# Kernel optimization log

Hardware: AMD Instinct MI355X
Metric: run time of the kernel (lower is better)

The kernel has to match this reference:

```python
import jax, jax.numpy as jnp
import numpy as np

DIM = 1024
NUM_EXPERTS = 8
TOP_K = 2
HIDDEN = int(2 * 4 * DIM / 3)  # 2730, SwiGLU hidden dim


def setup_inputs() -> dict:
    key = jax.random.key(0)
    ks = jax.random.split(key, 5)
    s = 0.02
    return {
        "x": jax.random.normal(ks[0], (2, 2048, DIM), dtype=jnp.float32),
        "router_w": jax.random.normal(ks[1], (DIM, NUM_EXPERTS), dtype=jnp.float32) * s,
        "w_gate": jax.random.normal(ks[2], (NUM_EXPERTS, DIM, HIDDEN), dtype=jnp.float32) * s,
        "w_up": jax.random.normal(ks[3], (NUM_EXPERTS, DIM, HIDDEN), dtype=jnp.float32) * s,
        "w_down": jax.random.normal(ks[4], (NUM_EXPERTS, HIDDEN, DIM), dtype=jnp.float32) * s,
    }


def reference(x, router_w, w_gate, w_up, w_down):
    B, S, D = x.shape
    xf = x.reshape(-1, D)  # [T, D]

    router_logits = xf @ router_w  # [T, E]
    topk_logits, topk_idx = jax.lax.top_k(router_logits, TOP_K)  # [T, K]
    routing_weights = jax.nn.softmax(topk_logits, axis=-1)  # [T, K]

    # Scatter top-k weights into dense [T, E] combine weights (0 for unselected
    # experts) -> mathematically identical to the per-expert gather/scatter loop.
    combine = (jax.nn.one_hot(topk_idx, NUM_EXPERTS, dtype=xf.dtype)
               * routing_weights[..., None]).sum(axis=1)  # [T, E]

    # SwiGLU experts computed for all tokens, weighted combine.
    gate = jax.nn.silu(jnp.einsum('td,edh->eth', xf, w_gate))  # [E, T, H]
    up = jnp.einsum('td,edh->eth', xf, w_up)                   # [E, T, H]
    expert_out = jnp.einsum('eth,ehd->etd', gate * up, w_down)  # [E, T, D]
    out = jnp.einsum('te,etd->td', combine, expert_out).reshape(B, S, D)

    # Auxiliary losses
    router_probs = jax.nn.softmax(router_logits, axis=-1)
    expert_usage = router_probs.mean(axis=0)
    load_balance_loss = NUM_EXPERTS * jnp.sum(expert_usage ** 2)
    router_z_loss = jnp.mean(jax.nn.logsumexp(router_logits, axis=-1) ** 2)
    return out, load_balance_loss, router_z_loss
```

## Files before the change

### kernel.cpp

```cpp
#include <hip/hip_runtime.h>
#include <cstdint>
#include <cstddef>

#define T_TOK 4096
#define DIM   1024
#define NEXP  8
#define HID   2730
#define HP2   2816
#define NB1   5632
#define NPAIR (T_TOK*2)

typedef __attribute__((ext_vector_type(8))) short short8;
typedef __attribute__((ext_vector_type(4))) float f32x4;

#define OFF_CNT   0UL
#define OFF_USE   64UL
#define OFF_Z     96UL
#define OFF_OFFS  160UL
#define OFF_LIST  256UL
#define OFF_PAIRW 131328UL
#define OFF_XB    164096UL
#define OFF_H     (OFF_XB + 8388608UL)
#define OFF_B2    (OFF_H + 46137344UL)
#define OFF_B1    (OFF_B2 + 46137344UL)
#define OFF_OP    OFF_B1

__device__ __forceinline__ unsigned short f2bf(float f) {
    unsigned u = __float_as_uint(f);
    return (unsigned short)((u + 0x7FFFu + ((u >> 16) & 1u)) >> 16);
}

__device__ __forceinline__ unsigned pack2(float a, float b) {
    return (unsigned)f2bf(a) | ((unsigned)f2bf(b) << 16);
}

__device__ __forceinline__ void load_lds16(const void* g, void* l) {
    __builtin_amdgcn_global_load_lds(
        (const __attribute__((address_space(1))) void*)g,
        (__attribute__((address_space(3))) void*)l, 16, 0, 0);
}

struct __align__(8) us4 { unsigned short x, y, z, w; };
struct __align__(8) u32x2 { unsigned x, y; };

__global__ __launch_bounds__(256) void router_kernel(
    const float* __restrict__ x, const float* __restrict__ rw,
    int* __restrict__ counts, float* __restrict__ usage, float* __restrict__ zacc,
    int* __restrict__ lists, float* __restrict__ pairw,
    unsigned short* __restrict__ xb)
{
    __shared__ float s_rw[NEXP][DIM];
    __shared__ float s_use[NEXP];
    __shared__ float s_z;
    const int tid = threadIdx.x;
    for (int i = tid; i < DIM * NEXP; i += 256) s_rw[i & 7][i >> 3] = rw[i];
    if (tid < NEXP) s_use[tid] = 0.f;
    if (tid == NEXP) s_z = 0.f;
    __syncthreads();

    const int wave = tid >> 6, lane = tid & 63;
    const int t = blockIdx.x * 4 + wave;

    float acc[NEXP];
    #pragma unroll
    for (int e = 0; e < NEXP; ++e) acc[e] = 0.f;
    #pragma unroll
    for (int j = 0; j < DIM / 64; ++j) {
        const int d = j * 64 + lane;
        const float xv = x[(size_t)t * DIM + d];
        xb[(size_t)t * DIM + d] = f2bf(xv);
        #pragma unroll
        for (int e = 0; e < NEXP; ++e) acc[e] = fmaf(xv, s_rw[e][d], acc[e]);
    }
    #pragma unroll
    for (int e = 0; e < NEXP; ++e) {
        float v = acc[e];
        for (int off = 32; off > 0; off >>= 1) v += __shfl_down(v, off, 64);
        acc[e] = v;
    }
    if (lane == 0) {
        float l[NEXP];
        #pragma unroll
        for (int e = 0; e < NEXP; ++e) l[e] = acc[e];
        float m = l[0];
        #pragma unroll
        for (int e = 1; e < NEXP; ++e) m = fmaxf(m, l[e]);
        float se = 0.f;
        #pragma unroll
        for (int e = 0; e < NEXP; ++e) se += __expf(l[e] - m);
        const float lse = m + __logf(se);
        #pragma unroll
        for (int e = 0; e < NEXP; ++e) atomicAdd(&s_use[e], __expf(l[e] - m) / se);
        atomicAdd(&s_z, lse * lse);
        int i0 = 0; float l0 = l[0];
        #pragma unroll
        for (int e = 1; e < NEXP; ++e) if (l[e] > l0) { l0 = l[e]; i0 = e; }
        int i1 = -1; float l1 = -1e30f;
        #pragma unroll
        for (int e = 0; e < NEXP; ++e) if (e != i0 && l[e] > l1) { l1 = l[e]; i1 = e; }
        const float p0 = 1.f / (1.f + __expf(l1 - l0));
        const float p1 = 1.f - p0;
        const int pos0 = atomicAdd(&counts[i0], 1);
        lists[i0 * T_TOK + pos0] = (t << 1);
        const int pos1 = atomicAdd(&counts[i1], 1);
        lists[i1 * T_TOK + pos1] = (t << 1) | 1;
        pairw[2 * t]     = p0;
        pairw[2 * t + 1] = p1;
    }
    __syncthreads();
    if (tid < NEXP) atomicAdd(&usage[tid], s_use[tid]);
    if (tid == NEXP) atomicAdd(zacc, s_z);
}

__global__ void finalize_kernel(const int* __restrict__ counts,
                                const float* __restrict__ usage,
                                const float* __restrict__ zacc,
                                int* __restrict__ offs,
                                float* __restrict__ out)
{
    if (threadIdx.x == 0 && blockIdx.x == 0) {
        int o = 0;
        for (int e = 0; e < NEXP; ++e) { offs[e] = o; o += counts[e]; }
        float s = 0.f;
        for (int e = 0; e < NEXP; ++e) {
            const float u = usage[e] / (float)T_TOK;
            s += u * u;
        }
        out[(size_t)T_TOK * DIM]     = (float)NEXP * s;
        out[(size_t)T_TOK * DIM + 1] = zacc[0] / (float)T_TOK;
    }
}

__global__ __launch_bounds__(256) void conv_w1_kernel(
    const float* __restrict__ wg, const float* __restrict__ wu,
    unsigned short* __restrict__ B1)
{
    __shared__ unsigned short lg[128 * 128];
    __shared__ unsigned short lu[128 * 128];
    const int e = blockIdx.z;
    const int h0 = blockIdx.x * 128;
    const int k0 = blockIdx.y * 128;
    const int tid = threadIdx.x;
    const size_t wb = (size_t)e * DIM * HID;

    const int hu = (tid & 31) * 4;
    const int kg = tid >> 5;
    const bool full = (h0 + 128 <= HID);

    #pragma unroll
    for (int uu = 0; uu < 4; ++uu) {
        const int kk = (kg * 4 + uu) * 4;
        f32x4 g[4], u[4];
        if (full) {
            #pragma unroll
            for (int j = 0; j < 4; ++j) {
                const size_t src = wb + (size_t)(k0 + kk + j) * HID + h0 + hu;
                g[j] = *(const f32x4*)&wg[src];
                u[j] = *(const f32x4*)&wu[src];
            }
        } else {
            #pragma unroll
            for (int j = 0; j < 4; ++j) {
                #pragma unroll
                for (int c = 0; c < 4; ++c) {
                    const int hh = h0 + hu + c;
                    float gv = 0.f, uv = 0.f;
                    if (hh < HID) {
                        const size_t src = wb + (size_t)(k0 + kk + j) * HID + hh;
                        gv = wg[src]; uv = wu[src];
                    }
                    g[j][c] = gv; u[j][c] = uv;
                }
            }
        }
        #pragma unroll
        for (int i = 0; i < 4; ++i) {
            const int h = hu + i;
            const int byte = (((h * 128 + kk) * 2) ^ ((h & 15) << 4));
            u32x2 vg; vg.x = pack2(g[0][i], g[1][i]); vg.y = pack2(g[2][i], g[3][i]);
            u32x2 vu; vu.x = pack2(u[0][i], u[1][i]); vu.y = pack2(u[2][i], u[3][i]);
            *(u32x2*)((char*)lg + byte) = vg;
            *(u32x2*)((char*)lu + byte) = vu;
        }
    }
    __syncthreads();

    const int kc  = (tid & 15) * 8;
    const int hrb = tid >> 4;
    #pragma unroll
    for (int wo = 0; wo < 8; ++wo) {
        const int h = hrb + wo * 16;
        const int byte = (((h * 128 + kc) * 2) ^ ((h & 15) << 4));
        const short8 vg = *(const short8*)((const char*)lg + byte);
        const short8 vu = *(const short8*)((const char*)lu + byte);
        *(short8*)&B1[((size_t)e * NB1 + h0 + h) * DIM + k0 + kc] = vg;
        *(short8*)&B1[((size_t)e * NB1 + HP2 + h0 + h) * DIM + k0 + kc] = vu;
    }
}

__global__ __launch_bounds__(256) void conv_w2_kernel(
    const float* __restrict__ wd, unsigned short* __restrict__ B2)
{
    __shared__ unsigned short lw[128 * 128];
    const int e = blockIdx.z;
    const int h0 = blockIdx.x * 128;
    const int d0 = blockIdx.y * 128;
    const int tid = threadIdx.x;
    const size_t wb = (size_t)e * HID * DIM;

    const int du = (tid & 31) * 4;
    const int kg = tid >> 5;

    #pragma unroll
    for (int uu = 0; uu < 4; ++uu) {
        const int kk = (kg * 4 + uu) * 4;
        f32x4 v[4];
        #pragma unroll
        for (int j = 0; j < 4; ++j) {
            const int hh = h0 + kk + j;
            if (hh < HID) v[j] = *(const f32x4*)&wd[wb + (size_t)hh * DIM + d0 + du];
            else          v[j] = (f32x4)0.f;
        }
        #pragma unroll
        for (int i = 0; i < 4; ++i) {
            const int d = du + i;
            const int byte = (((d * 128 + kk) * 2) ^ ((d & 15) << 4));
            u32x2 vv; vv.x = pack2(v[0][i], v[1][i]); vv.y = pack2(v[2][i], v[3][i]);
            *(u32x2*)((char*)lw + byte) = vv;
        }
    }
    __syncthreads();

    const int kc  = (tid & 15) * 8;
    const int drb = tid >> 4;
    #pragma unroll
    for (int wo = 0; wo < 8; ++wo) {
        const int d = drb + wo * 16;
        const int byte = (((d * 128 + kc) * 2) ^ ((d & 15) << 4));
        const short8 vv = *(const short8*)((const char*)lw + byte);
        *(short8*)&B2[((size_t)e * DIM + d0 + d) * HP2 + h0 + kc] = vv;
    }
}

__global__ __launch_bounds__(256, 2) void gemm1_kernel(
    const unsigned short* __restrict__ xb, const unsigned short* __restrict__ B1,
    const int* __restrict__ counts, const int* __restrict__ offs,
    const int* __restrict__ lists, unsigned short* __restrict__ h)
{
    const int e = blockIdx.z;
    const int cnt = counts[e];
    int wg = blockIdx.x + 22 * blockIdx.y;
    wg = (wg & 7) * 88 + (wg >> 3);
    const int by = wg & 31;
    const int bx = wg >> 5;
    const int row0 = by * 128;
    if (row0 >= cnt) return;
    const int off = offs[e];
    const int n0 = bx * 128;

    __shared__ unsigned short s1[24576];
    __shared__ int s_pr[128];

    const int tid = threadIdx.x;
    const int w = tid >> 6, lane = tid & 63;
    if (tid < 128) {
        const int r = row0 + tid;
        s_pr[tid] = (r < cnt) ? lists[e * T_TOK + r] : -1;
    }
    __syncthreads();

    const int rA = tid >> 2, kb = tid & 3;
    const int kbs = (kb ^ ((rA >> 1) & 3)) * 8;
    const int pr0 = s_pr[rA], pr1 = s_pr[rA + 64];
    const unsigned short* agp0 = xb + (size_t)(max(pr0, 0) >> 1) * DIM + kbs;
    const unsigned short* agp1 = xb + (size_t)(max(pr1, 0) >> 1) * DIM + kbs;
    const unsigned short* bgp0 = B1 + ((size_t)e * NB1 + n0 + rA) * DIM + kbs;
    const unsigned short* bgp1 = bgp0 + (size_t)64 * DIM;
    const unsigned short* bup0 = B1 + ((size_t)e * NB1 + HP2 + n0 + rA) * DIM + kbs;
    const unsigned short* bup1 = bup0 + (size_t)64 * DIM;

    char* const s1b = (char*)s1;
    const int sw = w * 1024;

    f32x4 accg[4][4], accu[4][4];
    #pragma unroll
    for (int i = 0; i < 4; ++i)
        #pragma unroll
        for (int j = 0; j < 4; ++j) { accg[i][j] = (f32x4)0.f; accu[i][j] = (f32x4)0.f; }

    const int wm = w & 1, wn = w >> 1;
    const int fm = lane & 15, fq = lane >> 4;
    const int kq = (fq ^ ((fm >> 1) & 3)) * 8;

    auto STAGE = [&](char* base, int k0) {
        load_lds16(agp0 + k0, base + sw);
        load_lds16(agp1 + k0, base + 4096 + sw);
        load_lds16(bgp0 + k0, base + 8192 + sw);
        load_lds16(bgp1 + k0, base + 12288 + sw);
        load_lds16(bup0 + k0, base + 16384 + sw);
        load_lds16(bup1 + k0, base + 20480 + sw);
    };
    auto COMPUTE = [&](const unsigned short* bufA) {
        const unsigned short* bufG = bufA + 4096;
        const unsigned short* bufU = bufA + 8192;
        short8 a[4], bg[4], bu[4];
        #pragma unroll
        for (int i = 0; i < 4; ++i) {
            a[i]  = *(const short8*)&bufA[(wm * 64 + i * 16 + fm) * 32 + kq];
            bg[i] = *(const short8*)&bufG[(wn * 64 + i * 16 + fm) * 32 + kq];
            bu[i] = *(const short8*)&bufU[(wn * 64 + i * 16 + fm) * 32 + kq];
        }
        __builtin_amdgcn_s_setprio(1);
        #pragma unroll
        for (int i = 0; i < 4; ++i)
            #pragma unroll
            for (int j = 0; j < 4; ++j) {
                accg[i][j] = __builtin_amdgcn_mfma_f32_16x16x32_bf16(a[i], bg[j], accg[i][j], 0, 0, 0);
                accu[i][j] = __builtin_amdgcn_mfma_f32_16x16x32_bf16(a[i], bu[j], accu[i][j], 0, 0, 0);
            }
        __builtin_amdgcn_s_setprio(0);
    };

    STAGE(s1b, 0);
    __syncthreads();
    #pragma unroll 1
    for (int g = 0; g < 16; ++g) {
        STAGE(s1b + 24576, g * 64 + 32);
        COMPUTE(s1);
        __syncthreads();
        if (g < 15) STAGE(s1b, g * 64 + 64);
        COMPUTE(s1 + 12288);
        __syncthreads();
    }

    unsigned short* wbuf = s1 + w * 1152;
    const int rrow = lane >> 2, cq = (lane & 3) * 16;
    #pragma unroll
    for (int i = 0; i < 4; ++i) {
        #pragma unroll
        for (int j = 0; j < 4; ++j)
            #pragma unroll
            for (int reg = 0; reg < 4; ++reg) {
                const float g = accg[i][j][reg];
                const float u = accu[i][j][reg];
                const float s = g / (1.f + __expf(-g));
                wbuf[(fq * 4 + reg) * 72 + j * 16 + fm] = f2bf(s * u);
            }
        const int rl = wm * 64 + i * 16 + rrow;
        if (row0 + rl < cnt) {
            unsigned short* dst = h + (size_t)(off + row0 + rl) * HP2 + n0 + wn * 64 + cq;
            const short8 v0 = *(const short8*)&wbuf[rrow * 72 + cq];
            const short8 v1 = *(const short8*)&wbuf[rrow * 72 + cq + 8];
            *(short8*)dst = v0;
            *(short8*)(dst + 8) = v1;
        }
    }
}

__global__ __launch_bounds__(256, 2) void gemm2_kernel(
    const unsigned short* __restrict__ h, const unsigned short* __restrict__ B2,
    const int* __restrict__ counts, const int* __restrict__ offs,
    const int* __restrict__ lists, unsigned short* __restrict__ op)
{
    const int e = blockIdx.z;
    const int cnt = counts[e];
    int wg = blockIdx.x + 8 * blockIdx.y;
    wg = (wg & 7) * 32 + (wg >> 3);
    const int by = wg & 31;
    const int bx = wg >> 5;
    const int row0 = by * 128;
    if (row0 >= cnt) return;
    const int off = offs[e];
    const int n0 = bx * 128;

    __shared__ unsigned short s2[32768];
    __shared__ int s_pr[128];

    const int tid = threadIdx.x;
    const int w = tid >> 6, lane = tid & 63;
    if (tid < 128) {
        const int r = row0 + tid;
        s_pr[tid] = (r < cnt) ? lists[e * T_TOK + r] : -1;
    }
    __syncthreads();

    const int rA = tid >> 2, kb = tid & 3;
    const int kbs = (kb ^ ((rA >> 1) & 3)) * 8;
    const unsigned short* agp0 = h + (size_t)(off + row0 + rA) * HP2 + kbs;
    const unsigned short* agp1 = agp0 + (size_t)64 * HP2;
    const unsigned short* bp0 = B2 + ((size_t)e * DIM + n0 + rA) * HP2 + kbs;
    const unsigned short* bp1 = bp0 + (size_t)64 * HP2;

    char* const s2b = (char*)s2;
    const int sw = w * 1024;

    f32x4 acc[4][4];
    #pragma unroll
    for (int i = 0; i < 4; ++i)
        #pragma unroll
        for (int j = 0; j < 4; ++j) acc[i][j] = (f32x4)0.f;

    const int wm = w & 1, wn = w >> 1;
    const int fm = lane & 15, fq = lane >> 4;
    const int kq = (fq ^ ((fm >> 1) & 3)) * 8;

    auto STAGE = [&](char* base, int k0) {
        load_lds16(agp0 + k0,      base + sw);
        load_lds16(agp1 + k0,      base + 4096 + sw);
        load_lds16(agp0 + k0 + 32, base + 8192 + sw);
        load_lds16(agp1 + k0 + 32, base + 12288 + sw);
        load_lds16(bp0 + k0,       base + 16384 + sw);
        load_lds16(bp1 + k0,       base + 20480 + sw);
        load_lds16(bp0 + k0 + 32,  base + 24576 + sw);
        load_lds16(bp1 + k0 + 32,  base + 28672 + sw);
    };
    auto COMPUTE = [&](const unsigned short* buf) {
        #pragma unroll
        for (int hh = 0; hh < 2; ++hh) {
            const unsigned short* bufA = buf + hh * 4096;
            const unsigned short* bufB = buf + 8192 + hh * 4096;
            short8 a[4], bb[4];
            #pragma unroll
            for (int i = 0; i < 4; ++i) {
                a[i]  = *(const short8*)&bufA[(wm * 64 + i * 16 + fm) * 32 + kq];
                bb[i] = *(const short8*)&bufB[(wn * 64 + i * 16 + fm) * 32 + kq];
            }
            __builtin_amdgcn_s_setprio(1);
            #pragma unroll
            for (int i = 0; i < 4; ++i)
                #pragma unroll
                for (int j = 0; j < 4; ++j)
                    acc[i][j] = __builtin_amdgcn_mfma_f32_16x16x32_bf16(a[i], bb[j], acc[i][j], 0, 0, 0);
            __builtin_amdgcn_s_setprio(0);
        }
    };

    STAGE(s2b, 0);
    __syncthreads();
    #pragma unroll 1
    for (int g = 0; g < 22; ++g) {
        STAGE(s2b + 32768, g * 128 + 64);
        COMPUTE(s2);
        __syncthreads();
        if (g < 21) STAGE(s2b, g * 128 + 128);
        COMPUTE(s2 + 16384);
        __syncthreads();
    }

    unsigned short* wbuf = s2 + w * 1152;
    const int rrow = lane >> 2, cq = (lane & 3) * 16;
    #pragma unroll
    for (int i = 0; i < 4; ++i) {
        #pragma unroll
        for (int j = 0; j < 4; ++j)
            #pragma unroll
            for (int reg = 0; reg < 4; ++reg)
                wbuf[(fq * 4 + reg) * 72 + j * 16 + fm] = f2bf(acc[i][j][reg]);
        const int rl = wm * 64 + i * 16 + rrow;
        const int pr = s_pr[rl];
        if (pr >= 0) {
            unsigned short* dst = op + (size_t)pr * DIM + n0 + wn * 64 + cq;
            const short8 v0 = *(const short8*)&wbuf[rrow * 72 + cq];
            const short8 v1 = *(const short8*)&wbuf[rrow * 72 + cq + 8];
            *(short8*)dst = v0;
            *(short8*)(dst + 8) = v1;
        }
    }
}

__global__ __launch_bounds__(256) void combine_kernel(
    const unsigned short* __restrict__ op, const float* __restrict__ pairw,
    float* __restrict__ out)
{
    const int f = blockIdx.x * 256 + threadIdx.x;
    const int t = f >> 8;
    const int c = f & 255;
    const float w0 = pairw[2 * t], w1 = pairw[2 * t + 1];
    const us4 a = ((const us4*)op)[(size_t)(2 * t) * (DIM / 4) + c];
    const us4 b = ((const us4*)op)[(size_t)(2 * t + 1) * (DIM / 4) + c];
    float4 r;
    r.x = w0 * __uint_as_float((unsigned)a.x << 16) + w1 * __uint_as_float((unsigned)b.x << 16);
    r.y = w0 * __uint_as_float((unsigned)a.y << 16) + w1 * __uint_as_float((unsigned)b.y << 16);
    r.z = w0 * __uint_as_float((unsigned)a.z << 16) + w1 * __uint_as_float((unsigned)b.z << 16);
    r.w = w0 * __uint_as_float((unsigned)a.w << 16) + w1 * __uint_as_float((unsigned)b.w << 16);
    ((float4*)out)[f] = r;
}

extern "C" void kernel_launch(void* const* d_in, const int* in_sizes, int n_in,
                              void* d_out, int out_size, void* d_ws, size_t ws_size,
                              hipStream_t stream)
{
    const float* x  = (const float*)d_in[0];
    const float* rw = (const float*)d_in[1];
    const float* wg = (const float*)d_in[2];
    const float* wu = (const float*)d_in[3];
    const float* wd = (const float*)d_in[4];
    float* out = (float*)d_out;
    char* ws = (char*)d_ws;

    int*   counts = (int*)(ws + OFF_CNT);
    float* usage  = (float*)(ws + OFF_USE);
    float* zacc   = (float*)(ws + OFF_Z);
    int*   offs   = (int*)(ws + OFF_OFFS);
    int*   lists  = (int*)(ws + OFF_LIST);
    float* pairw  = (float*)(ws + OFF_PAIRW);
    unsigned short* xb  = (unsigned short*)(ws + OFF_XB);
    unsigned short* hb  = (unsigned short*)(ws + OFF_H);
    unsigned short* B2  = (unsigned short*)(ws + OFF_B2);
    unsigned short* B1  = (unsigned short*)(ws + OFF_B1);
    unsigned short* op  = (unsigned short*)(ws + OFF_OP);

    hipMemsetAsync(ws, 0, 128, stream);

    router_kernel<<<T_TOK / 4, 256, 0, stream>>>(x, rw, counts, usage, zacc, lists, pairw, xb);
    finalize_kernel<<<1, 64, 0, stream>>>(counts, usage, zacc, offs, out);

    conv_w1_kernel<<<dim3(HP2 / 128, DIM / 128, NEXP), 256, 0, stream>>>(wg, wu, B1);
    conv_w2_kernel<<<dim3(HP2 / 128, DIM / 128, NEXP), 256, 0, stream>>>(wd, B2);

    gemm1_kernel<<<dim3(HP2 / 128, T_TOK / 128, NEXP), 256, 0, stream>>>(xb, B1, counts, offs, lists, hb);
    gemm2_kernel<<<dim3(DIM / 128, T_TOK / 128, NEXP), 256, 0, stream>>>(hb, B2, counts, offs, lists, op);

    combine_kernel<<<(T_TOK * DIM / 4) / 256, 256, 0, stream>>>(op, pairw, out);
}
```

Baseline: 628.3 us.

## Triple-buffer gemm2 LDS with K=32 stages and partial vmcnt waits

Restructures the down-projection GEMM main loop from double-buffered 64-wide K stages into a three-buffer ring of 32-wide K stages, shrinking LDS from 64KB to 48KB. Each step waits only for the older stage's loads (vmcnt(4)) before a raw barrier, so one prefetch stays in flight across the barrier. This aims to hide global-load latency better and may allow more resident blocks. In exchange there are more barriers per unit of K work, and correctness depends on the hand-counted vmcnt and the unrolled tail.

```diff
diff --git a/kernel.cpp b/kernel.cpp
--- a/kernel.cpp
+++ b/kernel.cpp
@@ -373,7 +373,7 @@
     const int off = offs[e];
     const int n0 = bx * 128;
 
-    __shared__ unsigned short s2[32768];
+    __shared__ unsigned short s2[24576];
     __shared__ int s_pr[128];
 
     const int tid = threadIdx.x;
@@ -405,47 +405,67 @@
     const int kq = (fq ^ ((fm >> 1) & 3)) * 8;
 
     auto STAGE = [&](char* base, int k0) {
-        load_lds16(agp0 + k0,      base + sw);
-        load_lds16(agp1 + k0,      base + 4096 + sw);
-        load_lds16(agp0 + k0 + 32, base + 8192 + sw);
-        load_lds16(agp1 + k0 + 32, base + 12288 + sw);
-        load_lds16(bp0 + k0,       base + 16384 + sw);
-        load_lds16(bp1 + k0,       base + 20480 + sw);
-        load_lds16(bp0 + k0 + 32,  base + 24576 + sw);
-        load_lds16(bp1 + k0 + 32,  base + 28672 + sw);
+        load_lds16(agp0 + k0, base + sw);
+        load_lds16(agp1 + k0, base + 4096 + sw);
+        load_lds16(bp0 + k0,  base + 8192 + sw);
+        load_lds16(bp1 + k0,  base + 12288 + sw);
     };
-    auto COMPUTE = [&](const unsigned short* buf) {
-        #pragma unroll
-        for (int hh = 0; hh < 2; ++hh) {
-            const unsigned short* bufA = buf + hh * 4096;
-            const unsigned short* bufB = buf + 8192 + hh * 4096;
-            short8 a[4], bb[4];
+    auto COMPUTE = [&](const unsigned short* bufA) {
+        const unsigned short* bufB = bufA + 4096;
+        short8 a[4], bb[4];
+        #pragma unroll
+        for (int i = 0; i < 4; ++i) {
+            a[i]  = *(const short8*)&bufA[(wm * 64 + i * 16 + fm) * 32 + kq];
+            bb[i] = *(const short8*)&bufB[(wn * 64 + i * 16 + fm) * 32 + kq];
+        }
+        __builtin_amdgcn_s_setprio(1);
+        #pragma unroll
+        for (int i = 0; i < 4; ++i)
             #pragma unroll
-            for (int i = 0; i < 4; ++i) {
-                a[i]  = *(const short8*)&bufA[(wm * 64 + i * 16 + fm) * 32 + kq];
-                bb[i] = *(const short8*)&bufB[(wn * 64 + i * 16 + fm) * 32 + kq];
-            }
-            __builtin_amdgcn_s_setprio(1);
-            #pragma unroll
-            for (int i = 0; i < 4; ++i)
-                #pragma unroll
-                for (int j = 0; j < 4; ++j)
-                    acc[i][j] = __builtin_amdgcn_mfma_f32_16x16x32_bf16(a[i], bb[j], acc[i][j], 0, 0, 0);
-            __builtin_amdgcn_s_setprio(0);
-        }
+            for (int j = 0; j < 4; ++j)
+                acc[i][j] = __builtin_amdgcn_mfma_f32_16x16x32_bf16(a[i], bb[j], acc[i][j], 0, 0, 0);
+        __builtin_amdgcn_s_setprio(0);
     };
 
     STAGE(s2b, 0);
-    __syncthreads();
+    STAGE(s2b + 16384, 32);
+    asm volatile("s_waitcnt vmcnt(4)" ::: "memory");
+    __builtin_amdgcn_s_barrier();
+
     #pragma unroll 1
-    for (int g = 0; g < 22; ++g) {
-        STAGE(s2b + 32768, g * 128 + 64);
+    for (int base = 0; base < 84; base += 3) {
+        const int k2 = (base + 2) * 32;
+        STAGE(s2b + 32768, k2);
         COMPUTE(s2);
-        __syncthreads();
-        if (g < 21) STAGE(s2b, g * 128 + 128);
+        asm volatile("s_waitcnt vmcnt(4)" ::: "memory");
+        __builtin_amdgcn_s_barrier();
+
+        STAGE(s2b, k2 + 32);
+        COMPUTE(s2 + 8192);
+        asm volatile("s_waitcnt vmcnt(4)" ::: "memory");
+        __builtin_amdgcn_s_barrier();
+
+        STAGE(s2b + 16384, k2 + 64);
         COMPUTE(s2 + 16384);
-        __syncthreads();
-    }
+        asm volatile("s_waitcnt vmcnt(4)" ::: "memory");
+        __builtin_amdgcn_s_barrier();
+    }
+    STAGE(s2b + 32768, 86 * 32);
+    COMPUTE(s2);
+    asm volatile("s_waitcnt vmcnt(4)" ::: "memory");
+    __builtin_amdgcn_s_barrier();
+
+    STAGE(s2b, 87 * 32);
+    COMPUTE(s2 + 8192);
+    asm volatile("s_waitcnt vmcnt(4)" ::: "memory");
+    __builtin_amdgcn_s_barrier();
+
+    COMPUTE(s2 + 16384);
+    asm volatile("s_waitcnt vmcnt(0)" ::: "memory");
+    __builtin_amdgcn_s_barrier();
+
+    COMPUTE(s2);
+    __builtin_amdgcn_s_barrier();
 
     unsigned short* wbuf = s2 + w * 1152;
     const int rrow = lane >> 2, cq = (lane & 3) * 16;
```

Result: no change. 633.6 us (+0.8%).

## Batch router atomics in shared memory and merge conversion/finalize kernels

Applied to the files above, without the earlier changes.

The router now processes 16 tokens per block, collecting per-expert list entries in shared memory and reserving global slots with one atomic per expert per block instead of per token. The finalize kernel and the two weight-conversion kernels are merged into one launch, with block (0,0,0) doing the offsets and loss finalization. This cuts kernel launches and global atomic contention. The trade-off is fewer router blocks, and the w2 blocks now carry a second, unused LDS buffer, which may lower occupancy.

```diff
diff --git a/kernel.cpp b/kernel.cpp
--- a/kernel.cpp
+++ b/kernel.cpp
@@ -52,73 +52,93 @@
     __shared__ float s_rw[NEXP][DIM];
     __shared__ float s_use[NEXP];
     __shared__ float s_z;
+    __shared__ int   s_cnt[NEXP];
+    __shared__ int   s_base[NEXP];
+    __shared__ int   s_items[NEXP][32];
     const int tid = threadIdx.x;
     for (int i = tid; i < DIM * NEXP; i += 256) s_rw[i & 7][i >> 3] = rw[i];
-    if (tid < NEXP) s_use[tid] = 0.f;
+    if (tid < NEXP) { s_use[tid] = 0.f; s_cnt[tid] = 0; }
     if (tid == NEXP) s_z = 0.f;
     __syncthreads();
 
     const int wave = tid >> 6, lane = tid & 63;
-    const int t = blockIdx.x * 4 + wave;
-
-    float acc[NEXP];
-    #pragma unroll
-    for (int e = 0; e < NEXP; ++e) acc[e] = 0.f;
-    #pragma unroll
-    for (int j = 0; j < DIM / 64; ++j) {
-        const int d = j * 64 + lane;
-        const float xv = x[(size_t)t * DIM + d];
-        xb[(size_t)t * DIM + d] = f2bf(xv);
-        #pragma unroll
-        for (int e = 0; e < NEXP; ++e) acc[e] = fmaf(xv, s_rw[e][d], acc[e]);
-    }
-    #pragma unroll
-    for (int e = 0; e < NEXP; ++e) {
-        float v = acc[e];
-        for (int off = 32; off > 0; off >>= 1) v += __shfl_down(v, off, 64);
-        acc[e] = v;
-    }
-    if (lane == 0) {
-        float l[NEXP];
-        #pragma unroll
-        for (int e = 0; e < NEXP; ++e) l[e] = acc[e];
-        float m = l[0];
-        #pragma unroll
-        for (int e = 1; e < NEXP; ++e) m = fmaxf(m, l[e]);
-        float se = 0.f;
-        #pragma unroll
-        for (int e = 0; e < NEXP; ++e) se += __expf(l[e] - m);
-        const float lse = m + __logf(se);
-        #pragma unroll
-        for (int e = 0; e < NEXP; ++e) atomicAdd(&s_use[e], __expf(l[e] - m) / se);
-        atomicAdd(&s_z, lse * lse);
-        int i0 = 0; float l0 = l[0];
-        #pragma unroll
-        for (int e = 1; e < NEXP; ++e) if (l[e] > l0) { l0 = l[e]; i0 = e; }
-        int i1 = -1; float l1 = -1e30f;
-        #pragma unroll
-        for (int e = 0; e < NEXP; ++e) if (e != i0 && l[e] > l1) { l1 = l[e]; i1 = e; }
-        const float p0 = 1.f / (1.f + __expf(l1 - l0));
-        const float p1 = 1.f - p0;
-        const int pos0 = atomicAdd(&counts[i0], 1);
-        lists[i0 * T_TOK + pos0] = (t << 1);
-        const int pos1 = atomicAdd(&counts[i1], 1);
-        lists[i1 * T_TOK + pos1] = (t << 1) | 1;
-        pairw[2 * t]     = p0;
-        pairw[2 * t + 1] = p1;
-    }
-    __syncthreads();
-    if (tid < NEXP) atomicAdd(&usage[tid], s_use[tid]);
+
+    #pragma unroll 1
+    for (int it = 0; it < 4; ++it) {
+        const int t = blockIdx.x * 16 + wave * 4 + it;
+        float acc[NEXP];
+        #pragma unroll
+        for (int e = 0; e < NEXP; ++e) acc[e] = 0.f;
+        #pragma unroll
+        for (int j = 0; j < DIM / 64; ++j) {
+            const int d = j * 64 + lane;
+            const float xv = x[(size_t)t * DIM + d];
+            xb[(size_t)t * DIM + d] = f2bf(xv);
+            #pragma unroll
+            for (int e = 0; e < NEXP; ++e) acc[e] = fmaf(xv, s_rw[e][d], acc[e]);
+        }
+        #pragma unroll
+        for (int e = 0; e < NEXP; ++e) {
+            float v = acc[e];
+            for (int off = 32; off > 0; off >>= 1) v += __shfl_down(v, off, 64);
+            acc[e] = v;
+        }
+        if (lane == 0) {
+            float l[NEXP];
+            #pragma unroll
+            for (int e = 0; e < NEXP; ++e) l[e] = acc[e];
+            float m = l[0];
+            #pragma unroll
+            for (int e = 1; e < NEXP; ++e) m = fmaxf(m, l[e]);
+            float se = 0.f;
+            #pragma unroll
+            for (int e = 0; e < NEXP; ++e) se += __expf(l[e] - m);
+            const float lse = m + __logf(se);
+            #pragma unroll
+            for (int e = 0; e < NEXP; ++e) atomicAdd(&s_use[e], __expf(l[e] - m) / se);
+            atomicAdd(&s_z, lse * lse);
+            int i0 = 0; float l0 = l[0];
+            #pragma unroll
+            for (int e = 1; e < NEXP; ++e) if (l[e] > l0) { l0 = l[e]; i0 = e; }
+            int i1 = -1; float l1 = -1e30f;
+            #pragma unroll
+            for (int e = 0; e < NEXP; ++e) if (e != i0 && l[e] > l1) { l1 = l[e]; i1 = e; }
+            const float p0 = 1.f / (1.f + __expf(l1 - l0));
+            const float p1 = 1.f - p0;
+            const int pos0 = atomicAdd(&s_cnt[i0], 1);
+            s_items[i0][pos0] = (t << 1);
+            const int pos1 = atomicAdd(&s_cnt[i1], 1);
+            s_items[i1][pos1] = (t << 1) | 1;
+            pairw[2 * t]     = p0;
+            pairw[2 * t + 1] = p1;
+        }
+    }
+    __syncthreads();
+    if (tid < NEXP) {
+        s_base[tid] = atomicAdd(&counts[tid], s_cnt[tid]);
+        atomicAdd(&usage[tid], s_use[tid]);
+    }
     if (tid == NEXP) atomicAdd(zacc, s_z);
-}
-
-__global__ void finalize_kernel(const int* __restrict__ counts,
-                                const float* __restrict__ usage,
-                                const float* __restrict__ zacc,
-                                int* __restrict__ offs,
-                                float* __restrict__ out)
+    __syncthreads();
+    {
+        const int e = tid >> 5, idx = tid & 31;
+        if (idx < s_cnt[e]) lists[e * T_TOK + s_base[e] + idx] = s_items[e][idx];
+    }
+}
+
+__global__ __launch_bounds__(256) void conv_kernel(
+    const float* __restrict__ wg, const float* __restrict__ wu,
+    const float* __restrict__ wd,
+    unsigned short* __restrict__ B1, unsigned short* __restrict__ B2,
+    const int* __restrict__ counts, const float* __restrict__ usage,
+    const float* __restrict__ zacc, int* __restrict__ offs,
+    float* __restrict__ out)
 {
-    if (threadIdx.x == 0 && blockIdx.x == 0) {
+    __shared__ unsigned short lga[128 * 128];
+    __shared__ unsigned short lub[128 * 128];
+    const int tid = threadIdx.x;
+
+    if (blockIdx.x == 0 && blockIdx.y == 0 && blockIdx.z == 0 && tid == 0) {
         int o = 0;
         for (int e = 0; e < NEXP; ++e) { offs[e] = o; o += counts[e]; }
         float s = 0.f;
@@ -129,116 +149,101 @@
         out[(size_t)T_TOK * DIM]     = (float)NEXP * s;
         out[(size_t)T_TOK * DIM + 1] = zacc[0] / (float)T_TOK;
     }
-}
-
-__global__ __launch_bounds__(256) void conv_w1_kernel(
-    const float* __restrict__ wg, const float* __restrict__ wu,
-    unsigned short* __restrict__ B1)
-{
-    __shared__ unsigned short lg[128 * 128];
-    __shared__ unsigned short lu[128 * 128];
-    const int e = blockIdx.z;
-    const int h0 = blockIdx.x * 128;
-    const int k0 = blockIdx.y * 128;
-    const int tid = threadIdx.x;
-    const size_t wb = (size_t)e * DIM * HID;
-
-    const int hu = (tid & 31) * 4;
-    const int kg = tid >> 5;
-    const bool full = (h0 + 128 <= HID);
-
-    #pragma unroll
-    for (int uu = 0; uu < 4; ++uu) {
-        const int kk = (kg * 4 + uu) * 4;
-        f32x4 g[4], u[4];
-        if (full) {
+
+    const int e = blockIdx.z & 7;
+    if (blockIdx.z < 8) {
+        const int h0 = blockIdx.x * 128;
+        const int k0 = blockIdx.y * 128;
+        const size_t wb = (size_t)e * DIM * HID;
+        const int hu = (tid & 31) * 4;
+        const int kg = tid >> 5;
+        const bool full = (h0 + 128 <= HID);
+
+        #pragma unroll
+        for (int uu = 0; uu < 4; ++uu) {
+            const int kk = (kg * 4 + uu) * 4;
+            f32x4 g[4], u[4];
+            if (full) {
+                #pragma unroll
+                for (int j = 0; j < 4; ++j) {
+                    const size_t src = wb + (size_t)(k0 + kk + j) * HID + h0 + hu;
+                    g[j] = *(const f32x4*)&wg[src];
+                    u[j] = *(const f32x4*)&wu[src];
+                }
+            } else {
+                #pragma unroll
+                for (int j = 0; j < 4; ++j) {
+                    #pragma unroll
+                    for (int c = 0; c < 4; ++c) {
+                        const int hh = h0 + hu + c;
+                        float gv = 0.f, uv = 0.f;
+                        if (hh < HID) {
+                            const size_t src = wb + (size_t)(k0 + kk + j) * HID + hh;
+                            gv = wg[src]; uv = wu[src];
+                        }
+                        g[j][c] = gv; u[j][c] = uv;
+                    }
+                }
+            }
+            #pragma unroll
+            for (int i = 0; i < 4; ++i) {
+                const int h = hu + i;
+                const int byte = (((h * 128 + kk) * 2) ^ ((h & 15) << 4));
+                u32x2 vg; vg.x = pack2(g[0][i], g[1][i]); vg.y = pack2(g[2][i], g[3][i]);
+                u32x2 vu; vu.x = pack2(u[0][i], u[1][i]); vu.y = pack2(u[2][i], u[3][i]);
+                *(u32x2*)((char*)lga + byte) = vg;
+                *(u32x2*)((char*)lub + byte) = vu;
+            }
+        }
+        __syncthreads();
+
+        const int kc  = (tid & 15) * 8;
+        const int hrb = tid >> 4;
+        #pragma unroll
+        for (int wo = 0; wo < 8; ++wo) {
+            const int h = hrb + wo * 16;
+            const int byte = (((h * 128 + kc) * 2) ^ ((h & 15) << 4));
+            const short8 vg = *(const short8*)((const char*)lga + byte);
+            const short8 vu = *(const short8*)((const char*)lub + byte);
+            *(short8*)&B1[((size_t)e * NB1 + h0 + h) * DIM + k0 + kc] = vg;
+            *(short8*)&B1[((size_t)e * NB1 + HP2 + h0 + h) * DIM + k0 + kc] = vu;
+        }
+    } else {
+        const int h0 = blockIdx.x * 128;
+        const int d0 = blockIdx.y * 128;
+        const size_t wb = (size_t)e * HID * DIM;
+        const int du = (tid & 31) * 4;
+        const int kg = tid >> 5;
+
+        #pragma unroll
+        for (int uu = 0; uu < 4; ++uu) {
+            const int kk = (kg * 4 + uu) * 4;
+            f32x4 v[4];
             #pragma unroll
             for (int j = 0; j < 4; ++j) {
-                const size_t src = wb + (size_t)(k0 + kk + j) * HID + h0 + hu;
-                g[j] = *(const f32x4*)&wg[src];
-                u[j] = *(const f32x4*)&wu[src];
-            }
-        } else {
-            #pragma unroll
-            for (int j = 0; j < 4; ++j) {
-                #pragma unroll
-                for (int c = 0; c < 4; ++c) {
-                    const int hh = h0 + hu + c;
-                    float gv = 0.f, uv = 0.f;
-                    if (hh < HID) {
-                        const size_t src = wb + (size_t)(k0 + kk + j) * HID + hh;
-                        gv = wg[src]; uv = wu[src];
-                    }
-                    g[j][c] = gv; u[j][c] = uv;
-                }
-            }
-        }
-        #pragma unroll
-        for (int i = 0; i < 4; ++i) {
-            const int h = hu + i;
-            const int byte = (((h * 128 + kk) * 2) ^ ((h & 15) << 4));
-            u32x2 vg; vg.x = pack2(g[0][i], g[1][i]); vg.y = pack2(g[2][i], g[3][i]);
-            u32x2 vu; vu.x = pack2(u[0][i], u[1][i]); vu.y = pack2(u[2][i], u[3][i]);
-            *(u32x2*)((char*)lg + byte) = vg;
-            *(u32x2*)((char*)lu + byte) = vu;
-        }
-    }
-    __syncthreads();
-
-    const int kc  = (tid & 15) * 8;
-    const int hrb = tid >> 4;
-    #pragma unroll
-    for (int wo = 0; wo < 8; ++wo) {
-        const int h = hrb + wo * 16;
-        const int byte = (((h * 128 + kc) * 2) ^ ((h & 15) << 4));
-        const short8 vg = *(const short8*)((const char*)lg + byte);
-        const short8 vu = *(const short8*)((const char*)lu + byte);
-        *(short8*)&B1[((size_t)e * NB1 + h0 + h) * DIM + k0 + kc] = vg;
-        *(short8*)&B1[((size_t)e * NB1 + HP2 + h0 + h) * DIM + k0 + kc] = vu;
-    }
-}
-
-__global__ __launch_bounds__(256) void conv_w2_kernel(
-    const float* __restrict__ wd, unsigned short* __restrict__ B2)
-{
-    __shared__ unsigned short lw[128 * 128];
-    const int e = blockIdx.z;
-    const int h0 = blockIdx.x * 128;
-    const int d0 = blockIdx.y * 128;
-    const int tid = threadIdx.x;
-    const size_t wb = (size_t)e * HID * DIM;
-
-    const int du = (tid & 31) * 4;
-    const int kg = tid >> 5;
-
-    #pragma unroll
-    for (int uu = 0; uu < 4; ++uu) {
-        const int kk = (kg * 4 + uu) * 4;
-        f32x4 v[4];
-        #pragma unroll
-        for (int j = 0; j < 4; ++j) {
-            const int hh = h0 + kk + j;
-            if (hh < HID) v[j] = *(const f32x4*)&wd[wb + (size_t)hh * DIM + d0 + du];
-            else          v[j] = (f32x4)0.f;
-        }
-        #pragma unroll
-        for (int i = 0; i < 4; ++i) {
-            const int d = du + i;
-            const int byte = (((d * 128 + kk) * 2) ^ ((d & 15) << 4));
-            u32x2 vv; vv.x = pack2(v[0][i], v[1][i]); vv.y = pack2(v[2][i], v[3][i]);
-            *(u32x2*)((char*)lw + byte) = vv;
-        }
-    }
-    __syncthreads();
-
-    const int kc  = (tid & 15) * 8;
-    const int drb = tid >> 4;
-    #pragma unroll
-    for (int wo = 0; wo < 8; ++wo) {
-        const int d = drb + wo * 16;
-        const int byte = (((d * 128 + kc) * 2) ^ ((d & 15) << 4));
-        const short8 vv = *(const short8*)((const char*)lw + byte);
-        *(short8*)&B2[((size_t)e * DIM + d0 + d) * HP2 + h0 + kc] = vv;
+                const int hh = h0 + kk + j;
+                if (hh < HID) v[j] = *(const f32x4*)&wd[wb + (size_t)hh * DIM + d0 + du];
+                else          v[j] = (f32x4)0.f;
+            }
+            #pragma unroll
+            for (int i = 0; i < 4; ++i) {
+                const int d = du + i;
+                const int byte = (((d * 128 + kk) * 2) ^ ((d & 15) << 4));
+                u32x2 vv; vv.x = pack2(v[0][i], v[1][i]); vv.y = pack2(v[2][i], v[3][i]);
+                *(u32x2*)((char*)lga + byte) = vv;
+            }
+        }
+        __syncthreads();
+
+        const int kc  = (tid & 15) * 8;
+        const int drb = tid >> 4;
+        #pragma unroll
+        for (int wo = 0; wo < 8; ++wo) {
+            const int d = drb + wo * 16;
+            const int byte = (((d * 128 + kc) * 2) ^ ((d & 15) << 4));
+            const short8 vv = *(const short8*)((const char*)lga + byte);
+            *(short8*)&B2[((size_t)e * DIM + d0 + d) * HP2 + h0 + kc] = vv;
+        }
     }
 }
 
@@ -512,11 +517,10 @@
 
     hipMemsetAsync(ws, 0, 128, stream);
 
-    router_kernel<<<T_TOK / 4, 256, 0, stream>>>(x, rw, counts, usage, zacc, lists, pairw, xb);
-    finalize_kernel<<<1, 64, 0, stream>>>(counts, usage, zacc, offs, out);
-
-    conv_w1_kernel<<<dim3(HP2 / 128, DIM / 128, NEXP), 256, 0, stream>>>(wg, wu, B1);
-    conv_w2_kernel<<<dim3(HP2 / 128, DIM / 128, NEXP), 256, 0, stream>>>(wd, B2);
+    router_kernel<<<T_TOK / 16, 256, 0, stream>>>(x, rw, counts, usage, zacc, lists, pairw, xb);
+
+    conv_kernel<<<dim3(HP2 / 128, DIM / 128, 2 * NEXP), 256, 0, stream>>>(
+        wg, wu, wd, B1, B2, counts, usage, zacc, offs, out);
 
     gemm1_kernel<<<dim3(HP2 / 128, T_TOK / 128, NEXP), 256, 0, stream>>>(xb, B1, counts, offs, lists, hb);
     gemm2_kernel<<<dim3(DIM / 128, T_TOK / 128, NEXP), 256, 0, stream>>>(hb, B2, counts, offs, lists, op);
```

Measured after the change: 535.9 us. -14.7%, faster.
